# Optimization experiments

Hardware: AMD Instinct MI355X
Metric: run time of the kernel (lower is better)

The kernel has to match this reference:

```python
import jax, jax.numpy as jnp
import numpy as np

EPS = 1e-06
SOUND_SPEED = 343.0
SUBBAND_EDGES = [500.0, 2000.0, 8000.0]
IS_SOUND_IDX = 0
RHO_IDX = 1
NUM_CANDIDATES = 64


def setup_inputs() -> dict:
    key = jax.random.key(0)
    ks = jax.random.split(key, 6)
    B, T, F, S, D = 16, 2048, 1025, 4, NUM_CANDIDATES
    phase = jax.random.normal(ks[0], (B, 1, T, F), dtype=jnp.float32)
    comb = jax.random.normal(ks[1], (B, 2, T, F), dtype=jnp.float32)
    scalar = jax.random.normal(ks[2], (B, T, S), dtype=jnp.float32)
    scalar_observed_mask = jax.random.uniform(ks[3], (B, T, S), dtype=jnp.float32)
    scalar_reliable_mask = jax.random.uniform(ks[4], (B, T, S), dtype=jnp.float32)
    stpacc = jax.random.normal(ks[5], (B, 1, T, D), dtype=jnp.float32)
    # STFT bin centers up to 24 kHz
    frequencies_hz = (jnp.arange(F, dtype=jnp.float32) * (24000.0 / (F - 1)))
    spacing_grid_hz = jnp.linspace(50.0, 1000.0, D, dtype=jnp.float32)
    return {
        'phase': phase, 'comb': comb, 'scalar': scalar,
        'scalar_observed_mask': scalar_observed_mask,
        'scalar_reliable_mask': scalar_reliable_mask,
        'stpacc': stpacc, 'frequencies_hz': frequencies_hz,
        'spacing_grid_hz': spacing_grid_hz,
    }


def _periodicity_basis(freq, spacing):
    # [D, F]: raised-cosine comb pattern for each candidate spacing
    pattern = 0.5 * (1.0 + jnp.cos(2.0 * np.pi * (freq[None, :] / jnp.maximum(spacing[:, None], 1e-06))))
    return pattern / jnp.maximum(pattern.mean(axis=-1, keepdims=True), EPS)


def _subband_masks(freq):
    # static boundaries: [min(f)] + edges + [max(f)+1]; all bands nonempty for this grid
    bounds = [jnp.min(freq)] + [jnp.float32(e) for e in SUBBAND_EDGES] + [jnp.max(freq) + 1.0]
    masks = [((freq >= lo) & (freq < hi)).astype(freq.dtype) for lo, hi in zip(bounds[:-1], bounds[1:])]
    return jnp.stack(masks, axis=0)  # [S_band, F]


def reference(phase, comb, scalar, scalar_observed_mask, scalar_reliable_mask,
              stpacc, frequencies_hz, spacing_grid_hz):
    freq = frequencies_hz.astype(phase.dtype)
    log_mag = phase[:, 0, :, :]                 # [B,T,F]
    smooth_d1 = comb[:, 0, :, :]
    abs_d1 = jnp.abs(comb[:, 1, :, :])
    log_mag_centered = log_mag - jnp.mean(log_mag, axis=-1, keepdims=True)
    trough = jax.nn.relu(-log_mag_centered)
    d1_strength = jax.nn.relu(abs_d1) + 0.25 * jax.nn.relu(jnp.abs(smooth_d1))
    trough = trough * (1.0 + d1_strength)
    trough = trough / jnp.maximum(jnp.mean(trough, axis=-1, keepdims=True), EPS)

    basis = _periodicity_basis(freq, spacing_grid_hz.astype(phase.dtype))  # [D,F]
    D, F = basis.shape
    periodic_score = jnp.einsum('btf,df->btd', trough, basis) / float(F)

    channels = [periodic_score]
    bands = _subband_masks(freq)                           # [Sb,F]
    denom = jnp.maximum(jnp.sum(bands, axis=-1), 1.0)      # [Sb]
    masked_basis = basis[None, :, :] * bands[:, None, :]   # [Sb,D,F]
    band_scores = jnp.einsum('btf,sdf->bstd', trough, masked_basis) / denom[None, :, None, None]
    channels += [band_scores[:, s] for s in range(bands.shape[0])]

    # stpacc projection (last dim already == D, no interpolation needed)
    stp = jax.nn.relu(stpacc[:, 0, :, :])
    stp = stp / jnp.maximum(jnp.mean(stp, axis=-1, keepdims=True), EPS)
    channels.append(stp)

    B, T = trough.shape[0], trough.shape[1]
    obs_quality = jnp.broadcast_to(jnp.mean(scalar_observed_mask, axis=-1, keepdims=True), (B, T, D))
    rel_quality = jnp.broadcast_to(jnp.mean(scalar_reliable_mask, axis=-1, keepdims=True), (B, T, D))
    channels.append(obs_quality)
    channels.append(rel_quality)

    is_sound = jnp.broadcast_to(jnp.clip(scalar[:, :, IS_SOUND_IDX:IS_SOUND_IDX + 1], 0.0, 1.0), (B, T, D))
    channels.append(is_sound)
    rho = jnp.broadcast_to(jnp.abs(jnp.clip(scalar[:, :, RHO_IDX:RHO_IDX + 1], -1.0, 1.0)), (B, T, D))
    channels.append(rho)

    raw_likelihood_seq = jnp.stack(channels, axis=-1)      # [B,T,D,10]
    raw_distance_logits_seq = jnp.mean(raw_likelihood_seq, axis=-1) * (0.5 + 0.5 * is_sound)

    distance_grid_cm = (100.0 * SOUND_SPEED) / (2.0 * jnp.maximum(spacing_grid_hz, 1e-06))
    return (raw_likelihood_seq, raw_distance_logits_seq,
            spacing_grid_hz.astype(phase.dtype), distance_grid_cm.astype(phase.dtype))
```

## Files before the change

### kernel.cpp

```cpp
#include <hip/hip_runtime.h>
#include <hip/hip_fp16.h>
#include <math.h>

#define Bn 16
#define Tn 2048
#define Fn 1025
#define KP 1056
#define KROW 1064
#define ROWS 16
#define NSLOT 7
#define Dn 64
#define EPSF 1e-6f

typedef __attribute__((ext_vector_type(8))) _Float16 f16x8;
typedef __attribute__((ext_vector_type(4))) _Float16 f16x4;
typedef __attribute__((ext_vector_type(4))) float f32x4;

__device__ inline float waveReduceSum(float v) {
#pragma unroll
  for (int off = 32; off > 0; off >>= 1) v += __shfl_xor(v, off, 64);
  return v;
}

__global__ __launch_bounds__(256) void prep_kernel(
    const float* __restrict__ freq, const float* __restrict__ spacing,
    _Float16* __restrict__ basisT, float* __restrict__ out2, float* __restrict__ out3) {
  __shared__ float wsum[4];
  const int d = blockIdx.x;
  const int tid = threadIdx.x;
  const float sp = fmaxf(spacing[d], 1e-6f);

  float pv[5];
  float lsum = 0.f;
#pragma unroll
  for (int it = 0; it < 5; ++it) {
    int f = tid + 256 * it;
    float p = 0.f;
    if (f < Fn) {
      double arg = 6.2831853071795864769 * (double)(freq[f] / sp);
      p = 0.5f * (1.0f + (float)cos(arg));
      lsum += p;
    }
    pv[it] = p;
  }
  float s = waveReduceSum(lsum);
  if ((tid & 63) == 0) wsum[tid >> 6] = s;
  __syncthreads();
  float inv = 1.0f / fmaxf((wsum[0] + wsum[1] + wsum[2] + wsum[3]) * (1.0f / 1025.0f), EPSF);

#pragma unroll
  for (int it = 0; it < 5; ++it) {
    int f = tid + 256 * it;
    if (f < KP) basisT[(size_t)d * KP + f] = (_Float16)(pv[it] * inv);
  }
  if (tid == 0) {
    out2[d] = spacing[d];
    out3[d] = 17150.0f / sp;
  }
}

__global__ __launch_bounds__(512) void fused_kernel(
    const float* __restrict__ phase, const float* __restrict__ comb,
    const _Float16* __restrict__ basisT,
    const float* __restrict__ scalar, const float* __restrict__ obs_m,
    const float* __restrict__ rel_m, const float* __restrict__ stpacc,
    float* __restrict__ out0, float* __restrict__ out1) {
  __shared__ _Float16 uLDS[ROWS * KROW];
  __shared__ float cumS[ROWS * NSLOT * 65];
  __shared__ float rowScale[ROWS];

  const int lane = threadIdx.x & 63;
  const int w = __builtin_amdgcn_readfirstlane(threadIdx.x >> 6);
  const int row0 = blockIdx.x * ROWS;

#pragma unroll 1
  for (int k2 = 0; k2 < 2; ++k2) {
    const int rl = 2 * w + k2;
    const int row = row0 + rl;
    const int b = row >> 11;
    const int t = row & 2047;
    const float* prow  = phase + (size_t)row * Fn;
    const float* c0row = comb + ((size_t)(b * 2 + 0) * Tn + t) * Fn;
    const float* c1row = comb + ((size_t)(b * 2 + 1) * Tn + t) * Fn;

    float4 pv[5], c0v[5], c1v[5];
#pragma unroll
    for (int it = 0; it < 5; ++it) {
      const int i = lane + 64 * it;
      if (i < 256) {
        pv[it]  = *(const float4*)(prow  + 4 * i);
        c0v[it] = *(const float4*)(c0row + 4 * i);
        c1v[it] = *(const float4*)(c1row + 4 * i);
      } else if (i == 256) {
        pv[it]  = make_float4(prow[1024],  0.f, 0.f, 0.f);
        c0v[it] = make_float4(c0row[1024], 0.f, 0.f, 0.f);
        c1v[it] = make_float4(c1row[1024], 0.f, 0.f, 0.f);
      } else {
        pv[it]  = make_float4(0.f, 0.f, 0.f, 0.f);
        c0v[it] = make_float4(0.f, 0.f, 0.f, 0.f);
        c1v[it] = make_float4(0.f, 0.f, 0.f, 0.f);
      }
    }

    float s = 0.f;
#pragma unroll
    for (int it = 0; it < 5; ++it)
      s += pv[it].x + pv[it].y + pv[it].z + pv[it].w;
    s = waveReduceSum(s);
    const float mean_lm = s * (1.0f / 1025.0f);

    _Float16* urow = uLDS + (size_t)rl * KROW;
    float su = 0.f;
#pragma unroll
    for (int it = 0; it < 5; ++it) {
      const int i = lane + 64 * it;
      float4 u;
      const float* pf = (const float*)&pv[it];
      const float* q0 = (const float*)&c0v[it];
      const float* q1 = (const float*)&c1v[it];
      float* uf = (float*)&u;
#pragma unroll
      for (int c2 = 0; c2 < 4; ++c2) {
        float tr = fmaxf(mean_lm - pf[c2], 0.f);
        float d1 = fabsf(q1[c2]) + 0.25f * fabsf(q0[c2]);
        uf[c2] = tr * (1.f + d1);
      }
      if (i > 256) { u.x = 0.f; u.y = 0.f; u.z = 0.f; u.w = 0.f; }
      else if (i == 256) { u.y = 0.f; u.z = 0.f; u.w = 0.f; }
      su += u.x + u.y + u.z + u.w;
      if (i < 264) {
        f16x4 hv;
#pragma unroll
        for (int c2 = 0; c2 < 4; ++c2) hv[c2] = (_Float16)uf[c2];
        *(f16x4*)(urow + 4 * i) = hv;
      }
    }
    su = waveReduceSum(su);
    if (lane == 0) rowScale[rl] = 1.0f / fmaxf(su * (1.0f / 1025.0f), EPSF);
  }
  __syncthreads();

  const int m16 = lane & 15;
  const int kg = lane >> 4;
  const int nh = w & 1;
  const int kq = w >> 1;
  const int d0 = nh * 32 + m16;

  const _Float16* ALp = uLDS + (size_t)m16 * KROW + kg * 8;
  const _Float16* B0 = basisT + (size_t)d0 * KP + kg * 8;
  const _Float16* B1 = basisT + (size_t)(d0 + 16) * KP + kg * 8;

  f32x4 acc0 = {0.f, 0.f, 0.f, 0.f};
  f32x4 acc1 = {0.f, 0.f, 0.f, 0.f};

  auto loadA = [&](int kt) { return *(const f16x8*)(ALp + kt * 32); };
  auto tileA = [&](int kt, f16x8 a) {
    f16x8 b0 = *(const f16x8*)(B0 + kt * 32);
    f16x8 b1 = *(const f16x8*)(B1 + kt * 32);
    acc0 = __builtin_amdgcn_mfma_f32_16x16x32_f16(a, b0, acc0, 0, 0, 0);
    acc1 = __builtin_amdgcn_mfma_f32_16x16x32_f16(a, b1, acc1, 0, 0, 0);
  };
  auto stor = [&](int slot, const f32x4& v0, const f32x4& v1) {
#pragma unroll
    for (int r = 0; r < 4; ++r) {
      const int rr = kg * 4 + r;
      cumS[(rr * NSLOT + slot) * 65 + d0]      = v0[r];
      cumS[(rr * NSLOT + slot) * 65 + d0 + 16] = v1[r];
    }
  };
  auto boundary = [&](int kt, int KB, f32x4& sa, f32x4& sb) {
    f16x8 a = loadA(kt);
    const int kb = kt * 32 + kg * 8;
    f16x8 alo, ahi;
#pragma unroll
    for (int j = 0; j < 8; ++j) {
      bool lo = (kb + j) < KB;
      alo[j] = lo ? a[j] : (_Float16)0.f;
      ahi[j] = lo ? (_Float16)0.f : a[j];
    }
    tileA(kt, alo);
    sa = acc0; sb = acc1;
    tileA(kt, ahi);
  };

  if (kq == 0) {
    f32x4 za = {0.f, 0.f, 0.f, 0.f};
    f32x4 s22a = za, s22b = za, s86a = za, s86b = za;
    boundary(0, 22, s22a, s22b);
    tileA(1, loadA(1));
    boundary(2, 86, s86a, s86b);
#pragma unroll
    for (int kt = 3; kt < 8; ++kt) tileA(kt, loadA(kt));
    stor(0, acc0, acc1);
    stor(4, s22a, s22b);
    stor(5, s86a, s86b);
  } else if (kq == 1) {
    f32x4 za = {0.f, 0.f, 0.f, 0.f};
    f32x4 s342a = za, s342b = za;
    tileA(8, loadA(8));
    tileA(9, loadA(9));
    boundary(10, 342, s342a, s342b);
#pragma unroll
    for (int kt = 11; kt < 17; ++kt) tileA(kt, loadA(kt));
    stor(1, acc0, acc1);
    stor(6, s342a, s342b);
  } else if (kq == 2) {
#pragma unroll
    for (int kt = 17; kt < 25; ++kt) tileA(kt, loadA(kt));
    stor(2, acc0, acc1);
  } else {
#pragma unroll
    for (int kt = 25; kt < 33; ++kt) tileA(kt, loadA(kt));
    stor(3, acc0, acc1);
  }
  __syncthreads();

#pragma unroll
  for (int k2 = 0; k2 < 2; ++k2) {
    const int rl = 2 * w + k2;
    const size_t bt = (size_t)(row0 + rl);
    const float rs = rowScale[rl];

    float sv = fmaxf(stpacc[bt * Dn + lane], 0.f);

    float q[NSLOT];
#pragma unroll
    for (int s2 = 0; s2 < NSLOT; ++s2)
      q[s2] = cumS[(rl * NSLOT + s2) * 65 + lane];

    float total = q[0] + q[1] + q[2] + q[3];
    float cum342 = q[0] + q[6];

    float ssum = waveReduceSum(sv);
    float stp = sv / fmaxf(ssum * (1.0f / 64.0f), EPSF);

    float4 scv = *(const float4*)(scalar + bt * 4);
    float4 om  = *(const float4*)(obs_m  + bt * 4);
    float4 rm  = *(const float4*)(rel_m  + bt * 4);
    float obs_q = (om.x + om.y + om.z + om.w) * 0.25f;
    float rel_q = (rm.x + rm.y + rm.z + rm.w) * 0.25f;
    float is_snd = fminf(fmaxf(scv.x, 0.f), 1.f);
    float rho = fabsf(fminf(fmaxf(scv.y, -1.f), 1.f));

    float c0 = total * rs * (1.0f / 1025.0f);
    float c1 = q[4] * rs * (1.0f / 22.0f);
    float c2 = (q[5] - q[4]) * rs * (1.0f / 64.0f);
    float c3 = (cum342 - q[5]) * rs * (1.0f / 256.0f);
    float c4 = (total - cum342) * rs * (1.0f / 683.0f);

    float mean10 = (c0 + c1 + c2 + c3 + c4 + stp + obs_q + rel_q + is_snd + rho) * 0.1f;
    float logit = mean10 * (0.5f + 0.5f * is_snd);

    float2* op = (float2*)(out0 + (bt * Dn + lane) * 10);
    op[0] = make_float2(c0, c1);
    op[1] = make_float2(c2, c3);
    op[2] = make_float2(c4, stp);
    op[3] = make_float2(obs_q, rel_q);
    op[4] = make_float2(is_snd, rho);
    out1[bt * Dn + lane] = logit;
  }
}

extern "C" void kernel_launch(void* const* d_in, const int* in_sizes, int n_in,
                              void* d_out, int out_size, void* d_ws, size_t ws_size,
                              hipStream_t stream) {
  const float* phase   = (const float*)d_in[0];
  const float* comb    = (const float*)d_in[1];
  const float* scalar  = (const float*)d_in[2];
  const float* obs_m   = (const float*)d_in[3];
  const float* rel_m   = (const float*)d_in[4];
  const float* stpacc  = (const float*)d_in[5];
  const float* freq    = (const float*)d_in[6];
  const float* spacing = (const float*)d_in[7];

  float* out  = (float*)d_out;
  float* out0 = out;
  float* out1 = out + (size_t)Bn * Tn * Dn * 10;
  float* out2 = out1 + (size_t)Bn * Tn * Dn;
  float* out3 = out2 + Dn;

  _Float16* basisT = (_Float16*)d_ws;

  prep_kernel<<<Dn, 256, 0, stream>>>(freq, spacing, basisT, out2, out3);
  fused_kernel<<<Bn * Tn / ROWS, 512, 0, stream>>>(
      phase, comb, basisT, scalar, obs_m, rel_m, stpacc, out0, out1);
}
```

Baseline: 118.5 us.

## Make each wave compute its own rows' full-K GEMM, removing block barriers

Each wave now runs the MFMA over the whole K range for its own two rows (padded into 16 rows, with only 2 of them useful) against all 64 basis columns. Before, four waves split K and wrote partial sums to shared memory. This removes both __syncthreads and the shared-memory row-scale exchange, and keeps prefix sums per wave, so waves run independently. The cost is about 8x redundant MFMA work and B-operand loads per wave, since most of the 16 M-rows are duplicates, plus longer serial K chains.

```diff
diff --git a/kernel.cpp b/kernel.cpp
--- a/kernel.cpp
+++ b/kernel.cpp
@@ -8,7 +8,6 @@
 #define KP 1056
 #define KROW 1064
 #define ROWS 16
-#define NSLOT 7
 #define Dn 64
 #define EPSF 1e-6f
 
@@ -66,15 +65,13 @@
     const float* __restrict__ rel_m, const float* __restrict__ stpacc,
     float* __restrict__ out0, float* __restrict__ out1) {
   __shared__ _Float16 uLDS[ROWS * KROW];
-  __shared__ float cumS[ROWS * NSLOT * 65];
-  __shared__ float rowScale[ROWS];
+  __shared__ float cumS[8][2][4][64];
 
   const int lane = threadIdx.x & 63;
   const int w = __builtin_amdgcn_readfirstlane(threadIdx.x >> 6);
   const int row0 = blockIdx.x * ROWS;
 
-#pragma unroll 1
-  for (int k2 = 0; k2 < 2; ++k2) {
+  auto trough = [&](int k2) -> float {
     const int rl = 2 * w + k2;
     const int row = row0 + rl;
     const int b = row >> 11;
@@ -136,39 +133,46 @@
       }
     }
     su = waveReduceSum(su);
-    if (lane == 0) rowScale[rl] = 1.0f / fmaxf(su * (1.0f / 1025.0f), EPSF);
-  }
-  __syncthreads();
+    return 1.0f / fmaxf(su * (1.0f / 1025.0f), EPSF);
+  };
+
+  const float rs0 = trough(0);
+  const float rs1 = trough(1);
+
+  asm volatile("s_waitcnt lgkmcnt(0)" ::: "memory");
+  __builtin_amdgcn_sched_barrier(0);
 
   const int m16 = lane & 15;
   const int kg = lane >> 4;
-  const int nh = w & 1;
-  const int kq = w >> 1;
-  const int d0 = nh * 32 + m16;
-
-  const _Float16* ALp = uLDS + (size_t)m16 * KROW + kg * 8;
-  const _Float16* B0 = basisT + (size_t)d0 * KP + kg * 8;
-  const _Float16* B1 = basisT + (size_t)(d0 + 16) * KP + kg * 8;
+  const _Float16* ALp = uLDS + (size_t)(2 * w + (m16 & 1)) * KROW + kg * 8;
+  const _Float16* B0 = basisT + (size_t)(m16)      * KP + kg * 8;
+  const _Float16* B1 = basisT + (size_t)(16 + m16) * KP + kg * 8;
+  const _Float16* B2 = basisT + (size_t)(32 + m16) * KP + kg * 8;
+  const _Float16* B3 = basisT + (size_t)(48 + m16) * KP + kg * 8;
 
   f32x4 acc0 = {0.f, 0.f, 0.f, 0.f};
-  f32x4 acc1 = {0.f, 0.f, 0.f, 0.f};
+  f32x4 acc1 = acc0, acc2 = acc0, acc3 = acc0;
 
   auto loadA = [&](int kt) { return *(const f16x8*)(ALp + kt * 32); };
-  auto tileA = [&](int kt, f16x8 a) {
-    f16x8 b0 = *(const f16x8*)(B0 + kt * 32);
-    f16x8 b1 = *(const f16x8*)(B1 + kt * 32);
-    acc0 = __builtin_amdgcn_mfma_f32_16x16x32_f16(a, b0, acc0, 0, 0, 0);
-    acc1 = __builtin_amdgcn_mfma_f32_16x16x32_f16(a, b1, acc1, 0, 0, 0);
-  };
-  auto stor = [&](int slot, const f32x4& v0, const f32x4& v1) {
-#pragma unroll
-    for (int r = 0; r < 4; ++r) {
-      const int rr = kg * 4 + r;
-      cumS[(rr * NSLOT + slot) * 65 + d0]      = v0[r];
-      cumS[(rr * NSLOT + slot) * 65 + d0 + 16] = v1[r];
-    }
-  };
-  auto boundary = [&](int kt, int KB, f32x4& sa, f32x4& sb) {
+  auto tile = [&](int kt, f16x8 a) {
+    acc0 = __builtin_amdgcn_mfma_f32_16x16x32_f16(a, *(const f16x8*)(B0 + kt * 32), acc0, 0, 0, 0);
+    acc1 = __builtin_amdgcn_mfma_f32_16x16x32_f16(a, *(const f16x8*)(B1 + kt * 32), acc1, 0, 0, 0);
+    acc2 = __builtin_amdgcn_mfma_f32_16x16x32_f16(a, *(const f16x8*)(B2 + kt * 32), acc2, 0, 0, 0);
+    acc3 = __builtin_amdgcn_mfma_f32_16x16x32_f16(a, *(const f16x8*)(B3 + kt * 32), acc3, 0, 0, 0);
+  };
+  auto spill = [&](int slot) {
+    if (lane < 16) {
+      cumS[w][0][slot][lane]      = acc0[0];
+      cumS[w][0][slot][16 + lane] = acc1[0];
+      cumS[w][0][slot][32 + lane] = acc2[0];
+      cumS[w][0][slot][48 + lane] = acc3[0];
+      cumS[w][1][slot][lane]      = acc0[1];
+      cumS[w][1][slot][16 + lane] = acc1[1];
+      cumS[w][1][slot][32 + lane] = acc2[1];
+      cumS[w][1][slot][48 + lane] = acc3[1];
+    }
+  };
+  auto boundary = [&](int kt, int KB, int slot) {
     f16x8 a = loadA(kt);
     const int kb = kt * 32 + kg * 8;
     f16x8 alo, ahi;
@@ -178,58 +182,34 @@
       alo[j] = lo ? a[j] : (_Float16)0.f;
       ahi[j] = lo ? (_Float16)0.f : a[j];
     }
-    tileA(kt, alo);
-    sa = acc0; sb = acc1;
-    tileA(kt, ahi);
-  };
-
-  if (kq == 0) {
-    f32x4 za = {0.f, 0.f, 0.f, 0.f};
-    f32x4 s22a = za, s22b = za, s86a = za, s86b = za;
-    boundary(0, 22, s22a, s22b);
-    tileA(1, loadA(1));
-    boundary(2, 86, s86a, s86b);
-#pragma unroll
-    for (int kt = 3; kt < 8; ++kt) tileA(kt, loadA(kt));
-    stor(0, acc0, acc1);
-    stor(4, s22a, s22b);
-    stor(5, s86a, s86b);
-  } else if (kq == 1) {
-    f32x4 za = {0.f, 0.f, 0.f, 0.f};
-    f32x4 s342a = za, s342b = za;
-    tileA(8, loadA(8));
-    tileA(9, loadA(9));
-    boundary(10, 342, s342a, s342b);
-#pragma unroll
-    for (int kt = 11; kt < 17; ++kt) tileA(kt, loadA(kt));
-    stor(1, acc0, acc1);
-    stor(6, s342a, s342b);
-  } else if (kq == 2) {
-#pragma unroll
-    for (int kt = 17; kt < 25; ++kt) tileA(kt, loadA(kt));
-    stor(2, acc0, acc1);
-  } else {
-#pragma unroll
-    for (int kt = 25; kt < 33; ++kt) tileA(kt, loadA(kt));
-    stor(3, acc0, acc1);
-  }
-  __syncthreads();
-
-#pragma unroll
-  for (int k2 = 0; k2 < 2; ++k2) {
+    tile(kt, alo);
+    spill(slot);
+    tile(kt, ahi);
+  };
+
+  boundary(0, 22, 0);
+  tile(1, loadA(1));
+  boundary(2, 86, 1);
+#pragma unroll
+  for (int kt = 3; kt < 10; ++kt) tile(kt, loadA(kt));
+  boundary(10, 342, 2);
+#pragma unroll
+  for (int kt = 11; kt < 33; ++kt) tile(kt, loadA(kt));
+  spill(3);
+
+  asm volatile("s_waitcnt lgkmcnt(0)" ::: "memory");
+  __builtin_amdgcn_sched_barrier(0);
+
+  auto EPI = [&](int k2, float rs) {
     const int rl = 2 * w + k2;
     const size_t bt = (size_t)(row0 + rl);
-    const float rs = rowScale[rl];
 
     float sv = fmaxf(stpacc[bt * Dn + lane], 0.f);
 
-    float q[NSLOT];
-#pragma unroll
-    for (int s2 = 0; s2 < NSLOT; ++s2)
-      q[s2] = cumS[(rl * NSLOT + s2) * 65 + lane];
-
-    float total = q[0] + q[1] + q[2] + q[3];
-    float cum342 = q[0] + q[6];
+    float s22   = cumS[w][k2][0][lane];
+    float s86   = cumS[w][k2][1][lane];
+    float s342  = cumS[w][k2][2][lane];
+    float total = cumS[w][k2][3][lane];
 
     float ssum = waveReduceSum(sv);
     float stp = sv / fmaxf(ssum * (1.0f / 64.0f), EPSF);
@@ -243,10 +223,10 @@
     float rho = fabsf(fminf(fmaxf(scv.y, -1.f), 1.f));
 
     float c0 = total * rs * (1.0f / 1025.0f);
-    float c1 = q[4] * rs * (1.0f / 22.0f);
-    float c2 = (q[5] - q[4]) * rs * (1.0f / 64.0f);
-    float c3 = (cum342 - q[5]) * rs * (1.0f / 256.0f);
-    float c4 = (total - cum342) * rs * (1.0f / 683.0f);
+    float c1 = s22 * rs * (1.0f / 22.0f);
+    float c2 = (s86 - s22) * rs * (1.0f / 64.0f);
+    float c3 = (s342 - s86) * rs * (1.0f / 256.0f);
+    float c4 = (total - s342) * rs * (1.0f / 683.0f);
 
     float mean10 = (c0 + c1 + c2 + c3 + c4 + stp + obs_q + rel_q + is_snd + rho) * 0.1f;
     float logit = mean10 * (0.5f + 0.5f * is_snd);
@@ -258,7 +238,9 @@
     op[3] = make_float2(obs_q, rel_q);
     op[4] = make_float2(is_snd, rho);
     out1[bt * Dn + lane] = logit;
-  }
+  };
+  EPI(0, rs0);
+  EPI(1, rs1);
 }
 
 extern "C" void kernel_launch(void* const* d_in, const int* in_sizes, int n_in,
```

New measurement: 229.0 us. 1.93x slower.
